# Optimization experiments

Hardware: AMD Instinct MI355X
Metric: run time of the kernel (lower is better)

Reference implementation:

```python
import jax, jax.numpy as jnp
import numpy as np

S = 32        # window size along the 'time' (intra-patch) axis
C = 32        # channels
P = 4         # patch_size; T = P**3 = 64 = 2*S


def setup_inputs() -> dict:
    key = jax.random.key(0)
    k1, k2, k3 = jax.random.split(key, 3)
    x = jax.random.normal(k1, (2, C, 96, 96, 96), dtype=jnp.float32)
    # nn.Linear(S*C, S*C): weight (out,in), bias (out,)
    W = jax.random.normal(k2, (S * C, S * C), dtype=jnp.float32) / np.float32(np.sqrt(S * C))
    b = jax.random.normal(k3, (S * C,), dtype=jnp.float32) * 0.01
    return {"x": x, "W": W, "b": b}


def reference(x, W, b):
    B, Cc, H, Wd, D = x.shape
    Hp, Wp, Dp = H // P, Wd // P, D // P
    T = P ** 3  # intra-patch token count
    # (B,C,H,W,D) -> (B,C,T,H',W',D') -> (B,H',W',D',T,C)
    xr = x.reshape(B, Cc, T, Hp, Wp, Dp).transpose(0, 3, 4, 5, 2, 1)
    # shift_window: circular roll along T by S//2
    xr = jnp.roll(xr, S // 2, axis=4)
    # group T into windows of S, dense linear over S*C
    xg = xr.reshape(B, Hp, Wp, Dp, T // S, S * Cc)
    y = jnp.einsum('bhwdgk,ok->bhwdgo', xg, W) + b
    # roll back by -(S//2)
    y = jnp.roll(y.reshape(B, Hp, Wp, Dp, T, Cc), -(S // 2), axis=4)
    # (B,H',W',D',T,C) -> (B,C,T,H',W',D') -> (B,C,H,W,D)
    out = y.transpose(0, 5, 4, 1, 2, 3).reshape(B, Cc, H, Wd, D)
    return out
```

## Files before the change

### kernel.cpp

```cpp
#include <hip/hip_runtime.h>


#define NSPAT 884736
#define QQ    13824
#define MTOT  55296
#define KK    1024
#define TS    8192

typedef __attribute__((ext_vector_type(4))) float f32x4;
typedef __attribute__((ext_vector_type(8))) short bf16x8;

__device__ __forceinline__ short f2bf(float f) {
  unsigned u = __builtin_bit_cast(unsigned, f);
  u += 0x7fff + ((u >> 16) & 1);
  return (short)(u >> 16);
}

__device__ __forceinline__ void async16(short* lds, const short* g) {
  __builtin_amdgcn_global_load_lds(
      (const __attribute__((address_space(1))) unsigned*)g,
      (__attribute__((address_space(3))) unsigned*)lds, 16, 0, 0);
}

__global__ __launch_bounds__(256)
void convert_w(const float* __restrict__ Wm, short* __restrict__ Wbf) {
  const int wb = blockIdx.x;
  const int tid = threadIdx.x;
  const int nt = wb >> 4;
  const int kt = wb & 15;
  const int n0 = nt * 128;
#pragma unroll
  for (int it = 0; it < 4; it++) {
    const int idx = it * 256 + tid;
    const int row = idx >> 3;
    const int oc  = idx & 7;
    const float* wsrc = Wm + (size_t)(n0 + row) * 1024 + kt * 64 + oc * 8;
    const f32x4 a = *(const f32x4*)(wsrc);
    const f32x4 b = *(const f32x4*)(wsrc + 4);
    bf16x8 f;
#pragma unroll
    for (int t = 0; t < 4; t++) { f[t] = f2bf(a[t]); f[t + 4] = f2bf(b[t]); }
    const int swz = (oc * 8) ^ ((row & 7) << 3);
    *(bf16x8*)(Wbf + (size_t)wb * TS + row * 64 + swz) = f;
  }
}

__global__ __launch_bounds__(256, 2)
void swin_fused(const float* __restrict__ x, const short* __restrict__ Bw,
                const float* __restrict__ bias, float* __restrict__ out) {
  __shared__ __align__(16) short As[128 * 64];
  __shared__ __align__(16) short Bs[128 * 64];

  const int b0 = blockIdx.x;
  const int logical = (b0 & 7) * 432 + (b0 >> 3);
  const int nt = logical & 7;
  const int mt = logical >> 3;
  const int seg = mt / 108;
  const int q0  = (mt - seg * 108) * 128;
  const int bb  = seg >> 1;
  const int g   = seg & 1;
  const int n0  = nt * 128;

  const int tid  = threadIdx.x;
  const int wv   = tid >> 6;
  const int lane = tid & 63;
  const int wr   = wv >> 1;
  const int wc   = wv & 1;
  const int lm   = lane & 15;
  const int quad = lane >> 4;

  const int rg = tid >> 3;
  const int oc = tid & 7;
  const int jp = oc >> 2;
  const int cb = (oc & 3) * 8;
  const float* xbase = x + ((size_t)bb * 32 + cb) * NSPAT + q0 + rg * 4;
  int awof[4];
#pragma unroll
  for (int r = 0; r < 4; r++) {
    const int row = rg * 4 + r;
    awof[r] = row * 64 + ((oc * 8) ^ ((row & 7) << 3));
  }

  const short* bT = Bw + (size_t)nt * 16 * TS + wv * 2048 + lane * 8;
  short* bL = Bs + wv * 2048;

  const int rsw = (lm & 7) << 3;

  f32x4 acc[4][4];
#pragma unroll
  for (int i = 0; i < 4; i++)
#pragma unroll
    for (int jj = 0; jj < 4; jj++) {
      f32x4 z = {0.f, 0.f, 0.f, 0.f};
      acc[i][jj] = z;
    }

  for (int kt = 0; kt < 16; kt++) {
#pragma unroll
    for (int is = 0; is < 4; is++)
      async16(bL + is * 512, bT + (size_t)kt * TS + is * 512);

    const int tsrc = ((g << 5) + (kt << 1) + jp + 48) & 63;
    const float* src = xbase + (size_t)tsrc * QQ;
    bf16x8 o[4];
#pragma unroll
    for (int tt = 0; tt < 8; tt++) {
      const f32x4 v = *(const f32x4*)(src + (size_t)tt * NSPAT);
#pragma unroll
      for (int r = 0; r < 4; r++) o[r][tt] = f2bf(v[r]);
    }
#pragma unroll
    for (int r = 0; r < 4; r++)
      *(bf16x8*)(As + awof[r]) = o[r];

    __syncthreads();

#pragma unroll
    for (int ks = 0; ks < 2; ks++) {
      bf16x8 af[4], bfr[4];
#pragma unroll
      for (int i = 0; i < 4; i++)
        af[i] = *(const bf16x8*)(As + (wr * 64 + i * 16 + lm) * 64
                                    + ((ks * 32 + quad * 8) ^ rsw));
#pragma unroll
      for (int jj = 0; jj < 4; jj++)
        bfr[jj] = *(const bf16x8*)(Bs + (wc * 64 + jj * 16 + lm) * 64
                                      + ((ks * 32 + quad * 8) ^ rsw));
#pragma unroll
      for (int i = 0; i < 4; i++)
#pragma unroll
        for (int jj = 0; jj < 4; jj++)
          acc[i][jj] = __builtin_amdgcn_mfma_f32_16x16x32_bf16(af[i], bfr[jj], acc[i][jj], 0, 0, 0);
    }
    __syncthreads();
  }

  float* ob = out + (size_t)bb * 32 * NSPAT;
#pragma unroll
  for (int jj = 0; jj < 4; jj++) {
    const int o  = n0 + wc * 64 + jj * 16 + lm;
    const float bv = bias[o];
    const int so = o >> 5;
    const int cc = o & 31;
    const int tt = ((g << 5) + so + 48) & 63;
    float* orow = ob + (size_t)cc * NSPAT + (size_t)tt * QQ + q0;
#pragma unroll
    for (int i = 0; i < 4; i++) {
      const int mb = wr * 64 + i * 16 + quad * 4;
      f32x4 v = acc[i][jj];
      v += bv;
      *(f32x4*)(orow + mb) = v;
    }
  }
}

__global__ __launch_bounds__(256, 2)
void swin_gemm(const float* __restrict__ x, const float* __restrict__ Wm,
               const float* __restrict__ bias, float* __restrict__ out) {
  const int bid = blockIdx.x;
  const int nt  = bid & 7;
  const int mt  = bid >> 3;
  const int seg = mt / 108;
  const int q0  = (mt - seg * 108) * 128;
  const int bb  = seg >> 1;
  const int g   = seg & 1;

  const int tid  = threadIdx.x;
  const int wv   = tid >> 6;
  const int wr   = wv >> 1;
  const int wc   = wv & 1;
  const int lane = tid & 63;
  const int lm   = lane & 15;
  const int quad = lane >> 4;

  const int n0 = nt * 128 + wc * 64;

  int aoff[4];
#pragma unroll
  for (int i = 0; i < 4; i++)
    aoff[i] = (quad * 8) * NSPAT + q0 + wr * 64 + i * 16 + lm;

  const float* wptr[4];
#pragma unroll
  for (int j = 0; j < 4; j++)
    wptr[j] = Wm + (size_t)(n0 + j * 16 + lm) * 1024 + quad * 8;

  f32x4 acc[4][4];
#pragma unroll
  for (int i = 0; i < 4; i++)
#pragma unroll
    for (int j = 0; j < 4; j++) {
      f32x4 z = {0.f, 0.f, 0.f, 0.f};
      acc[i][j] = z;
    }

  const float* xb = x + (size_t)bb * 32 * NSPAT;

  for (int kc = 0; kc < 32; kc++) {
    const int t_src = ((g << 5) + kc + 48) & 63;
    const float* xs = xb + (size_t)t_src * QQ;

    bf16x8 af[4];
#pragma unroll
    for (int i = 0; i < 4; i++) {
      float v[8];
#pragma unroll
      for (int t = 0; t < 8; t++)
        v[t] = xs[aoff[i] + t * NSPAT];
      bf16x8 f;
#pragma unroll
      for (int t = 0; t < 8; t++) f[t] = f2bf(v[t]);
      af[i] = f;
    }

    bf16x8 bfr[4];
#pragma unroll
    for (int j = 0; j < 4; j++) {
      const float* wp = wptr[j] + kc * 32;
      const f32x4 w0 = *(const f32x4*)(wp);
      const f32x4 w1 = *(const f32x4*)(wp + 4);
      bf16x8 f;
#pragma unroll
      for (int t = 0; t < 4; t++) { f[t] = f2bf(w0[t]); f[t + 4] = f2bf(w1[t]); }
      bfr[j] = f;
    }

#pragma unroll
    for (int i = 0; i < 4; i++)
#pragma unroll
      for (int j = 0; j < 4; j++)
        acc[i][j] = __builtin_amdgcn_mfma_f32_16x16x32_bf16(af[i], bfr[j], acc[i][j], 0, 0, 0);
  }

  float* ob = out + (size_t)bb * 32 * NSPAT;
#pragma unroll
  for (int j = 0; j < 4; j++) {
    const int o  = n0 + j * 16 + lm;
    const float bv = bias[o];
    const int so = o >> 5;
    const int cc = o & 31;
    const int tt = ((g << 5) + so + 48) & 63;
    float* orow = ob + (size_t)cc * NSPAT + (size_t)tt * QQ + q0;
#pragma unroll
    for (int i = 0; i < 4; i++) {
      const int mb = wr * 64 + i * 16 + quad * 4;
      f32x4 v = acc[i][j];
      v += bv;
      *(f32x4*)(orow + mb) = v;
    }
  }
}

extern "C" void kernel_launch(void* const* d_in, const int* in_sizes, int n_in,
                              void* d_out, int out_size, void* d_ws, size_t ws_size,
                              hipStream_t stream) {
  const float* x    = (const float*)d_in[0];
  const float* Wm   = (const float*)d_in[1];
  const float* bias = (const float*)d_in[2];
  float* out        = (float*)d_out;

  const size_t need = (size_t)KK * KK * 2;
  if (ws_size >= need) {
    short* Wbf = (short*)d_ws;
    convert_w<<<dim3(128), dim3(256), 0, stream>>>(Wm, Wbf);
    swin_fused<<<dim3(432 * 8), dim3(256), 0, stream>>>(x, Wbf, bias, out);
  } else {
    swin_gemm<<<dim3(432 * 8), dim3(256), 0, stream>>>(x, Wm, bias, out);
  }
}
```

Before: 567.1 us.

## Software-pipeline fused GEMM with double-buffered A and triple-buffered B in LDS

The main loop of the fused kernel now prefetches the next K-tile of x into registers and issues async global-to-LDS loads for the W tile two steps ahead. It then runs the MFMA work on the current buffers. A uses two LDS buffers and B uses three, which removes one of the two barriers per iteration and hides global load latency behind compute. In exchange, LDS use per block rises from 32KB to 80KB, which could limit occupancy, and register pressure grows from the prefetched values.

```diff
diff --git a/kernel.cpp b/kernel.cpp
--- a/kernel.cpp
+++ b/kernel.cpp
@@ -48,8 +48,8 @@
 __global__ __launch_bounds__(256, 2)
 void swin_fused(const float* __restrict__ x, const short* __restrict__ Bw,
                 const float* __restrict__ bias, float* __restrict__ out) {
-  __shared__ __align__(16) short As[128 * 64];
-  __shared__ __align__(16) short Bs[128 * 64];
+  __shared__ __align__(16) short AsBuf[2 * 8192];
+  __shared__ __align__(16) short BsBuf[3 * 8192];
 
   const int b0 = blockIdx.x;
   const int logical = (b0 & 7) * 432 + (b0 >> 3);
@@ -82,7 +82,6 @@
   }
 
   const short* bT = Bw + (size_t)nt * 16 * TS + wv * 2048 + lane * 8;
-  short* bL = Bs + wv * 2048;
 
   const int rsw = (lm & 7) << 3;
 
@@ -95,44 +94,79 @@
       acc[i][jj] = z;
     }
 
+  f32x4 pre[8];
+  {
+    const int tsrc = ((g << 5) + jp + 48) & 63;
+    const float* src = xbase + (size_t)tsrc * QQ;
+#pragma unroll
+    for (int tt = 0; tt < 8; tt++) pre[tt] = *(const f32x4*)(src + (size_t)tt * NSPAT);
+  }
+#pragma unroll
+  for (int is = 0; is < 4; is++) async16(BsBuf + wv * 2048 + is * 512, bT + is * 512);
+#pragma unroll
+  for (int is = 0; is < 4; is++) async16(BsBuf + 8192 + wv * 2048 + is * 512, bT + TS + is * 512);
+  {
+    bf16x8 o[4];
+#pragma unroll
+    for (int tt = 0; tt < 8; tt++) {
+      const f32x4 v = pre[tt];
+#pragma unroll
+      for (int r = 0; r < 4; r++) o[r][tt] = f2bf(v[r]);
+    }
+#pragma unroll
+    for (int r = 0; r < 4; r++) *(bf16x8*)(AsBuf + awof[r]) = o[r];
+  }
+  asm volatile("s_waitcnt vmcnt(4) lgkmcnt(0)" ::: "memory");
+  __builtin_amdgcn_s_barrier();
+
   for (int kt = 0; kt < 16; kt++) {
-#pragma unroll
-    for (int is = 0; is < 4; is++)
-      async16(bL + is * 512, bT + (size_t)kt * TS + is * 512);
-
-    const int tsrc = ((g << 5) + (kt << 1) + jp + 48) & 63;
-    const float* src = xbase + (size_t)tsrc * QQ;
-    bf16x8 o[4];
-#pragma unroll
-    for (int tt = 0; tt < 8; tt++) {
-      const f32x4 v = *(const f32x4*)(src + (size_t)tt * NSPAT);
-#pragma unroll
-      for (int r = 0; r < 4; r++) o[r][tt] = f2bf(v[r]);
-    }
-#pragma unroll
-    for (int r = 0; r < 4; r++)
-      *(bf16x8*)(As + awof[r]) = o[r];
-
-    __syncthreads();
-
+    if (kt < 15) {
+      const int tsrc = ((g << 5) + ((kt + 1) << 1) + jp + 48) & 63;
+      const float* src = xbase + (size_t)tsrc * QQ;
+#pragma unroll
+      for (int tt = 0; tt < 8; tt++) pre[tt] = *(const f32x4*)(src + (size_t)tt * NSPAT);
+    }
+    if (kt < 14) {
+      short* bW = BsBuf + ((kt + 2) % 3) * 8192 + wv * 2048;
+      const short* bgs = bT + (size_t)(kt + 2) * TS;
+#pragma unroll
+      for (int is = 0; is < 4; is++) async16(bW + is * 512, bgs + is * 512);
+    }
+
+    const short* asC = AsBuf + (kt & 1) * 8192;
+    const short* bsC = BsBuf + (kt % 3) * 8192;
 #pragma unroll
     for (int ks = 0; ks < 2; ks++) {
       bf16x8 af[4], bfr[4];
 #pragma unroll
       for (int i = 0; i < 4; i++)
-        af[i] = *(const bf16x8*)(As + (wr * 64 + i * 16 + lm) * 64
-                                    + ((ks * 32 + quad * 8) ^ rsw));
+        af[i] = *(const bf16x8*)(asC + (wr * 64 + i * 16 + lm) * 64
+                                     + ((ks * 32 + quad * 8) ^ rsw));
 #pragma unroll
       for (int jj = 0; jj < 4; jj++)
-        bfr[jj] = *(const bf16x8*)(Bs + (wc * 64 + jj * 16 + lm) * 64
-                                      + ((ks * 32 + quad * 8) ^ rsw));
+        bfr[jj] = *(const bf16x8*)(bsC + (wc * 64 + jj * 16 + lm) * 64
+                                       + ((ks * 32 + quad * 8) ^ rsw));
 #pragma unroll
       for (int i = 0; i < 4; i++)
 #pragma unroll
         for (int jj = 0; jj < 4; jj++)
           acc[i][jj] = __builtin_amdgcn_mfma_f32_16x16x32_bf16(af[i], bfr[jj], acc[i][jj], 0, 0, 0);
     }
-    __syncthreads();
+
+    if (kt < 15) {
+      bf16x8 o[4];
+#pragma unroll
+      for (int tt = 0; tt < 8; tt++) {
+        const f32x4 v = pre[tt];
+#pragma unroll
+        for (int r = 0; r < 4; r++) o[r][tt] = f2bf(v[r]);
+      }
+      short* asN = AsBuf + ((kt + 1) & 1) * 8192;
+#pragma unroll
+      for (int r = 0; r < 4; r++) *(bf16x8*)(asN + awof[r]) = o[r];
+      asm volatile("s_waitcnt vmcnt(4) lgkmcnt(0)" ::: "memory");
+      __builtin_amdgcn_s_barrier();
+    }
   }
 
   float* ob = out + (size_t)bb * 32 * NSPAT;
```

New measurement: 613.1 us. 8.1% more time.
